# Optimization experiments

Measured on AMD Instinct MI355X. Metric: run time of the kernel, lower is better.

## Reference

```python
import jax, jax.numpy as jnp
import numpy as np
import math

N_BINS = 100  # len(torch.arange(0.01, 1.01, 0.01))


def _soft_histogram_masks(H, W, dtype=jnp.float32):
    # radial distance from image center, 'ij' meshgrid like torch.meshgrid default
    a = jnp.arange(H, dtype=dtype)[:, None]   # rows
    b = jnp.arange(W, dtype=dtype)[None, :]   # cols
    dist = jnp.sqrt((a - H / 2) ** 2 + (b - W / 2) ** 2)  # [H, W]
    max_radius = math.sqrt(H * H + W * W) / 2
    radius_factors = jnp.arange(1, N_BINS + 1, dtype=dtype) * 0.01  # 0.01 .. 1.00
    radius_set = max_radius * radius_factors                        # [100]
    # s[i] = sigmoid(r_i - dist); bin mask i = s[i] - s[i-1], mask 0 = s[0]
    s = jax.nn.sigmoid(radius_set[:, None, None] - dist[None])      # [100, H, W]
    masks = s - jnp.concatenate([jnp.zeros((1, H, W), dtype), s[:-1]], axis=0)
    return masks  # [100, H, W]


def setup_inputs() -> dict:
    key = jax.random.key(0)
    k1, k2 = jax.random.split(key)
    B, C, H, W = 16, 3, 512, 512
    x = jax.random.normal(k1, (B, C, H, W), dtype=jnp.float32)
    value_set = jax.random.uniform(k2, (B, N_BINS), dtype=jnp.float32)
    return {"x": x, "value_set": value_set}


def reference(x, value_set):
    B, C, H, W = x.shape
    fq_mask_set = _soft_histogram_masks(H, W, x.dtype)           # [100, H, W]
    # weighted sum over bins; avoids materializing [B, 100, H, W]
    fq_mask = jnp.einsum('br,rhw->bhw', value_set, fq_mask_set)  # [B, H, W]
    return (fq_mask, value_set)
```

## Files before the change

kernel.cpp:

```cpp
#include <hip/hip_runtime.h>
#include <math.h>

#define HDIM   512
#define WDIM   512
#define BATCH  16
#define NBINS  100
#define NPIX   (HDIM * WDIM)

#define STEP      3.6203867196751236f
#define INV_STEP  0.27621358640099516f
#define CUT       8.0f
#define VSTRIDE   20

__device__ __forceinline__ float4 fma4(float a, float4 m, float4 c) {
    c.x = fmaf(a, m.x, c.x);
    c.y = fmaf(a, m.y, c.y);
    c.z = fmaf(a, m.z, c.z);
    c.w = fmaf(a, m.w, c.w);
    return c;
}

__global__ __launch_bounds__(256) void fq_mask_kernel(
    const float* __restrict__ value_set,
    float* __restrict__ out_mask,
    float* __restrict__ out_vs)
{
    __shared__ __align__(16) float vst[NBINS * VSTRIDE];
    const int tid = threadIdx.x;
    for (int i = tid; i < BATCH * NBINS; i += 256) {
        int b = i / NBINS;
        int r = i - b * NBINS;
        vst[r * VSTRIDE + b] = value_set[i];
    }
    __syncthreads();

    const int lane   = tid & 63;
    const int wv     = tid >> 6;
    const int row_in = wv * 8 + (lane >> 3);
    const int col_in = (lane & 7) * 4;
    const int by = blockIdx.x >> 4;
    const int bx = blockIdx.x & 15;
    const int h  = by * 32 + row_in;
    const int w  = bx * 32 + col_in;

    const float fy  = (float)h - 256.0f;
    const float dy2 = fy * fy;
    float d[4];
    #pragma unroll
    for (int p = 0; p < 4; ++p) {
        float dx = (float)(w + p) - 256.0f;
        d[p] = sqrtf(dy2 + dx * dx);
    }
    const float dmin = fminf(fminf(d[0], d[1]), fminf(d[2], d[3]));
    const float dmax = fmaxf(fmaxf(d[0], d[1]), fmaxf(d[2], d[3]));
    int r_lo = (int)floorf((dmin - CUT) * INV_STEP); if (r_lo < 0) r_lo = 0;
    int r_hi = (int)floorf((dmax + CUT) * INV_STEP); if (r_hi > NBINS - 1) r_hi = NBINS - 1;
    const int cnt = r_hi - r_lo + 1;

    const float dec = __expf(-STEP);
    float e[4], sp[4];
    #pragma unroll
    for (int p = 0; p < 4; ++p) {
        e[p]  = __expf(d[p] - STEP * (float)(r_lo + 1));
        sp[p] = 0.0f;
    }

    float4 acc[BATCH];
    #pragma unroll
    for (int b = 0; b < BATCH; ++b) acc[b] = make_float4(0.f, 0.f, 0.f, 0.f);

    int r = r_lo;
    for (int i = 0; i < cnt; ++i, ++r) {
        float mm[4];
        #pragma unroll
        for (int p = 0; p < 4; ++p) {
            float s = __builtin_amdgcn_rcpf(1.0f + e[p]);
            mm[p]  = s - sp[p];
            sp[p]  = s;
            e[p]  *= dec;
        }
        const float4 m = make_float4(mm[0], mm[1], mm[2], mm[3]);
        const float4* vr = (const float4*)&vst[r * VSTRIDE];
        #pragma unroll
        for (int c = 0; c < 4; ++c) {
            float4 v = vr[c];
            acc[4*c + 0] = fma4(v.x, m, acc[4*c + 0]);
            acc[4*c + 1] = fma4(v.y, m, acc[4*c + 1]);
            acc[4*c + 2] = fma4(v.z, m, acc[4*c + 2]);
            acc[4*c + 3] = fma4(v.w, m, acc[4*c + 3]);
        }
    }

    const int pixbase = h * WDIM + w;
    #pragma unroll
    for (int b = 0; b < BATCH; ++b)
        *(float4*)&out_mask[b * NPIX + pixbase] = acc[b];

    if (blockIdx.x == 0) {
        for (int i = tid; i < BATCH * NBINS; i += 256)
            out_vs[i] = value_set[i];
    }
}

extern "C" void kernel_launch(void* const* d_in, const int* in_sizes, int n_in,
                              void* d_out, int out_size, void* d_ws, size_t ws_size,
                              hipStream_t stream) {
    const float* value_set = (const float*)d_in[1];
    float* out_mask = (float*)d_out;
    float* out_vs   = (float*)d_out + BATCH * NPIX;

    const int threads = 256;
    const int blocks  = (HDIM / 32) * (WDIM / 32);
    fq_mask_kernel<<<blocks, threads, 0, stream>>>(value_set, out_mask, out_vs);
}
```

Baseline: 11.81 us.

## Split batch across blocks to raise grid parallelism and cut registers

The batch dimension is now split into groups of four, each handled by its own block, so the grid grows from 256 to 1024 blocks and each thread keeps 4 float4 accumulators instead of 16. This is meant to raise occupancy and spread work over more CUs than the 256-block grid could. The cost is recomputing the per-pixel distances and sigmoid recurrences four times, once per batch group.

```diff
diff --git a/kernel.cpp b/kernel.cpp
--- a/kernel.cpp
+++ b/kernel.cpp
@@ -6,11 +6,11 @@
 #define BATCH  16
 #define NBINS  100
 #define NPIX   (HDIM * WDIM)
+#define BG     4
 
 #define STEP      3.6203867196751236f
 #define INV_STEP  0.27621358640099516f
 #define CUT       8.0f
-#define VSTRIDE   20
 
 __device__ __forceinline__ float4 fma4(float a, float4 m, float4 c) {
     c.x = fmaf(a, m.x, c.x);
@@ -25,12 +25,14 @@
     float* __restrict__ out_mask,
     float* __restrict__ out_vs)
 {
-    __shared__ __align__(16) float vst[NBINS * VSTRIDE];
-    const int tid = threadIdx.x;
-    for (int i = tid; i < BATCH * NBINS; i += 256) {
-        int b = i / NBINS;
-        int r = i - b * NBINS;
-        vst[r * VSTRIDE + b] = value_set[i];
+    const int bg   = blockIdx.x >> 8;
+    const int tile = blockIdx.x & 255;
+    const int tid  = threadIdx.x;
+
+    __shared__ __align__(16) float vst[NBINS * BG];
+    for (int i = tid; i < NBINS * BG; i += 256) {
+        int r = i >> 2, j = i & 3;
+        vst[i] = value_set[(bg * BG + j) * NBINS + r];
     }
     __syncthreads();
 
@@ -38,8 +40,8 @@
     const int wv     = tid >> 6;
     const int row_in = wv * 8 + (lane >> 3);
     const int col_in = (lane & 7) * 4;
-    const int by = blockIdx.x >> 4;
-    const int bx = blockIdx.x & 15;
+    const int by = tile >> 4;
+    const int bx = tile & 15;
     const int h  = by * 32 + row_in;
     const int w  = bx * 32 + col_in;
 
@@ -65,10 +67,11 @@
         sp[p] = 0.0f;
     }
 
-    float4 acc[BATCH];
+    float4 acc[BG];
     #pragma unroll
-    for (int b = 0; b < BATCH; ++b) acc[b] = make_float4(0.f, 0.f, 0.f, 0.f);
+    for (int j = 0; j < BG; ++j) acc[j] = make_float4(0.f, 0.f, 0.f, 0.f);
 
+    const float4* vr = (const float4*)vst;
     int r = r_lo;
     for (int i = 0; i < cnt; ++i, ++r) {
         float mm[4];
@@ -80,21 +83,17 @@
             e[p]  *= dec;
         }
         const float4 m = make_float4(mm[0], mm[1], mm[2], mm[3]);
-        const float4* vr = (const float4*)&vst[r * VSTRIDE];
-        #pragma unroll
-        for (int c = 0; c < 4; ++c) {
-            float4 v = vr[c];
-            acc[4*c + 0] = fma4(v.x, m, acc[4*c + 0]);
-            acc[4*c + 1] = fma4(v.y, m, acc[4*c + 1]);
-            acc[4*c + 2] = fma4(v.z, m, acc[4*c + 2]);
-            acc[4*c + 3] = fma4(v.w, m, acc[4*c + 3]);
-        }
+        float4 v = vr[r];
+        acc[0] = fma4(v.x, m, acc[0]);
+        acc[1] = fma4(v.y, m, acc[1]);
+        acc[2] = fma4(v.z, m, acc[2]);
+        acc[3] = fma4(v.w, m, acc[3]);
     }
 
     const int pixbase = h * WDIM + w;
     #pragma unroll
-    for (int b = 0; b < BATCH; ++b)
-        *(float4*)&out_mask[b * NPIX + pixbase] = acc[b];
+    for (int j = 0; j < BG; ++j)
+        *(float4*)&out_mask[(bg * BG + j) * NPIX + pixbase] = acc[j];
 
     if (blockIdx.x == 0) {
         for (int i = tid; i < BATCH * NBINS; i += 256)
@@ -110,6 +109,6 @@
     float* out_vs   = (float*)d_out + BATCH * NPIX;
 
     const int threads = 256;
-    const int blocks  = (HDIM / 32) * (WDIM / 32);
+    const int blocks  = (BATCH / BG) * (HDIM / 32) * (WDIM / 32);
     fq_mask_kernel<<<blocks, threads, 0, stream>>>(value_set, out_mask, out_vs);
 }
```

Result: faster. 11.14 us (-5.7%).
